# Performance work log

Hardware: AMD Instinct MI355X
Metric: run time of the kernel (lower is better)

Reference implementation:

```python
import jax, jax.numpy as jnp
import numpy as np

NUM_HEADS = 8
NG = 8  # group/grid size: seq = NG**3 = 512


def setup_inputs() -> dict:
    key = jax.random.key(0)
    k1, k2, k3 = jax.random.split(key, 3)
    batch, seq, chan = 32, NG ** 3, 512
    subspace_dim = 24
    x = jax.random.normal(k1, (batch, seq, chan), jnp.float32)
    # fixed symmetric-subspace basis (the free variable `conv_kernel` in the source)
    basis = jax.random.normal(k2, (seq, subspace_dim), jnp.float32)
    # learned param: (subspace_dim, num_heads), init stddev 0.01
    kernel = jax.random.normal(k3, (subspace_dim, NUM_HEADS), jnp.float32) * 0.01
    return {"x": x, "basis": basis, "kernel": kernel}


def reference(x, basis, kernel):
    batch, seq, chan = x.shape
    h, ng = NUM_HEADS, NG
    kn = 2 * ng - 1  # 15: circular tiling window
    ch = chan // h
    # 'batch (8 8 8) (ch h) -> h (batch ch) 8 8 8'
    x_im = x.reshape(batch, ng, ng, ng, ch, h)
    x_im = jnp.transpose(x_im, (5, 0, 4, 1, 2, 3)).reshape(h, batch * ch, ng, ng, ng)
    # circular tiling: tile 2x2x2 then crop to 2*ng-1 per axis; add trailing C=1
    x_im = jnp.tile(x_im, (1, 1, 2, 2, 2))[:, :, :kn, :kn, :kn, None]
    # expand subspace kernel: '(n n n) s, s h -> h n n n 1 1'
    kexp = jnp.einsum('gs,sh->hg', basis, kernel).reshape(h, ng, ng, ng, 1, 1)

    def conv(lhs, rhs):
        return jax.lax.conv_general_dilated(
            lhs, rhs, window_strides=(1, 1, 1), padding='VALID',
            dimension_numbers=('NXYZC', 'XYZIO', 'NXYZC'))

    # per-head VALID conv: [batch*ch, 15,15,15, 1] * [8,8,8,1,1] -> [batch*ch, 8,8,8, 1]
    out = jax.vmap(conv)(x_im, kexp)[..., 0]  # [h, batch*ch, 8, 8, 8]
    # 'h (batch ch) n n n -> batch (n n n) (ch h)'
    out = out.reshape(h, batch, ch, seq)
    out = jnp.transpose(out, (1, 3, 2, 0)).reshape(batch, seq, chan)
    return out
```

## Files before the change

### kernel.cpp

```cpp
#include <hip/hip_runtime.h>


#define S2C 0.70710678118654752f
#define S2  18
#define S1  146
#define CST 1172

template <bool INV>
__device__ __forceinline__ void dft8(float* R, float* I)
{
    float t0r = R[0] + R[4], t0i = I[0] + I[4];
    float t1r = R[1] + R[5], t1i = I[1] + I[5];
    float t2r = R[2] + R[6], t2i = I[2] + I[6];
    float t3r = R[3] + R[7], t3i = I[3] + I[7];
    float b0r = R[0] - R[4], b0i = I[0] - I[4];
    float d1r = R[1] - R[5], d1i = I[1] - I[5];
    float d2r = R[2] - R[6], d2i = I[2] - I[6];
    float d3r = R[3] - R[7], d3i = I[3] - I[7];
    float b1r, b1i, b2r, b2i, b3r, b3i;
    if (!INV) {
        b1r = (d1r + d1i) * S2C;  b1i = (d1i - d1r) * S2C;
        b2r = d2i;                b2i = -d2r;
        b3r = (d3i - d3r) * S2C;  b3i = -(d3r + d3i) * S2C;
    } else {
        b1r = (d1r - d1i) * S2C;  b1i = (d1i + d1r) * S2C;
        b2r = -d2i;               b2i = d2r;
        b3r = -(d3r + d3i) * S2C; b3i = (d3r - d3i) * S2C;
    }
    float u0r = t0r + t2r, u0i = t0i + t2i;
    float u1r = t1r + t3r, u1i = t1i + t3i;
    float u2r = t0r - t2r, u2i = t0i - t2i;
    float e3r = t1r - t3r, e3i = t1i - t3i;
    float u3r, u3i;
    if (!INV) { u3r = e3i;  u3i = -e3r; }
    else      { u3r = -e3i; u3i = e3r;  }
    R[0] = u0r + u1r; I[0] = u0i + u1i;
    R[4] = u0r - u1r; I[4] = u0i - u1i;
    R[2] = u2r + u3r; I[2] = u2i + u3i;
    R[6] = u2r - u3r; I[6] = u2i - u3i;
    float v0r = b0r + b2r, v0i = b0i + b2i;
    float v1r = b1r + b3r, v1i = b1i + b3i;
    float v2r = b0r - b2r, v2i = b0i - b2i;
    float w3r = b1r - b3r, w3i = b1i - b3i;
    float v3r, v3i;
    if (!INV) { v3r = w3i;  v3i = -w3r; }
    else      { v3r = -w3i; v3i = w3r;  }
    R[1] = v0r + v1r; I[1] = v0i + v1i;
    R[5] = v0r - v1r; I[5] = v0i - v1i;
    R[3] = v2r + v3r; I[3] = v2i + v3i;
    R[7] = v2r - v3r; I[7] = v2i - v3i;
}

__device__ const float CTAB8[8] = {1.f, S2C, 0.f, -S2C, -1.f, -S2C, 0.f, S2C};
__device__ const float STAB8[8] = {0.f, S2C, 1.f, S2C, 0.f, -S2C, -1.f, -S2C};

__global__ __launch_bounds__(256)
void eqfft_prep(const float* __restrict__ basis,
                const float* __restrict__ kparam,
                float2* __restrict__ V)
{
    __shared__ float Wl[512];
    __shared__ float CT[8], ST[8];
    const int tid = threadIdx.x;
    const int blk = blockIdx.x;
    const int h   = blk >> 4;
    if (tid < 8) { CT[tid] = CTAB8[tid]; ST[tid] = STAB8[tid]; }
    #pragma unroll
    for (int t = 0; t < 2; ++t) {
        const int g = tid * 2 + t;
        const float* bp = basis + g * 24;
        float acc = 0.f;
        #pragma unroll
        for (int s = 0; s < 24; ++s) acc += bp[s] * kparam[s * 8 + h];
        Wl[(g & 63) * 8 + (g >> 6)] = acc;
    }
    __syncthreads();
    const int f  = (blk & 15) * 32 + (tid >> 3);
    const int g1 = tid & 7;
    const int f1 = f >> 6, f2 = (f >> 3) & 7, f3 = f & 7;
    const int kb = (f1 * g1) & 7;
    float pr = 0.f, pi = 0.f;
    for (int g2 = 0; g2 < 8; ++g2) {
        const int k2 = kb + f2 * g2;
        const float* wrow = &Wl[g2 * 64 + g1];
        #pragma unroll
        for (int g3 = 0; g3 < 8; ++g3) {
            const int k = (k2 + f3 * g3) & 7;
            const float w = wrow[g3 * 8];
            pr += w * CT[k];
            pi += w * ST[k];
        }
    }
    pr += __shfl_xor(pr, 1); pi += __shfl_xor(pi, 1);
    pr += __shfl_xor(pr, 2); pi += __shfl_xor(pi, 2);
    pr += __shfl_xor(pr, 4); pi += __shfl_xor(pi, 4);
    if (g1 == 0)
        V[h * 512 + f] = make_float2(pr * (1.f / 512.f), pi * (1.f / 512.f));
}

__global__ __launch_bounds__(256, 4)
void eqfft_main(const float* __restrict__ x,
                const float2* __restrict__ V,
                float* __restrict__ out)
{
    __shared__ __align__(16) float lds[8 * CST];

    const int tid = threadIdx.x;
    const int bid = blockIdx.x;
    const int b   = bid >> 5;
    const int c0  = (bid & 31) * 16;

    const float* xb = x   + (size_t)b * 262144 + c0;
    float*       ob = out + (size_t)b * 262144 + c0;

    #pragma unroll
    for (int t = 0; t < 4; ++t) {
        const int G = t * 256 + tid;
        const int p = G >> 1;
        const int u = G & 1;
        const float4 A  = *(const float4*)(xb + p * 512 + u * 4);
        const float4 Bv = *(const float4*)(xb + p * 512 + u * 4 + 8);
        const int base = (p >> 6) * S1 + ((p >> 3) & 7) * S2 + (p & 7) * 2;
        float* dst = lds + (u * 4) * CST + base;
        *(float2*)(dst + 0 * CST) = make_float2(A.x, Bv.x);
        *(float2*)(dst + 1 * CST) = make_float2(A.y, Bv.y);
        *(float2*)(dst + 2 * CST) = make_float2(A.z, Bv.z);
        *(float2*)(dst + 3 * CST) = make_float2(A.w, Bv.w);
    }
    __syncthreads();

    const int q = tid >> 5;
    const int e = tid & 31;
    float R0[8], I0[8], R1[8], I1[8];

    {
        const int P0 = 2 * e, P1 = 2 * e + 1;
        float* pa = lds + q * CST + (P0 >> 3) * S1 + (P0 & 7) * S2;
        float* pb = lds + q * CST + (P1 >> 3) * S1 + (P1 & 7) * S2;
        #pragma unroll
        for (int j = 0; j < 8; ++j) {
            const float2 za = *(const float2*)(pa + 2 * j);
            const float2 zb = *(const float2*)(pb + 2 * j);
            R0[j] = za.x; I0[j] = za.y; R1[j] = zb.x; I1[j] = zb.y;
        }
        dft8<false>(R0, I0); dft8<false>(R1, I1);
        #pragma unroll
        for (int j = 0; j < 8; ++j) {
            *(float2*)(pa + 2 * j) = make_float2(R0[j], I0[j]);
            *(float2*)(pb + 2 * j) = make_float2(R1[j], I1[j]);
        }
    }
    __syncthreads();

    {
        const int P0 = 2 * e, P1 = 2 * e + 1;
        float* pa = lds + q * CST + (P0 >> 3) * S1 + (P0 & 7) * 2;
        float* pb = lds + q * CST + (P1 >> 3) * S1 + (P1 & 7) * 2;
        #pragma unroll
        for (int j = 0; j < 8; ++j) {
            const float2 za = *(const float2*)(pa + S2 * j);
            const float2 zb = *(const float2*)(pb + S2 * j);
            R0[j] = za.x; I0[j] = za.y; R1[j] = zb.x; I1[j] = zb.y;
        }
        dft8<false>(R0, I0); dft8<false>(R1, I1);
        #pragma unroll
        for (int j = 0; j < 8; ++j) {
            *(float2*)(pa + S2 * j) = make_float2(R0[j], I0[j]);
            *(float2*)(pb + S2 * j) = make_float2(R1[j], I1[j]);
        }
    }
    __syncthreads();

    {
        const int P0 = 2 * e, P1 = 2 * e + 1;
        const int p2a = P0 >> 3, p3a = P0 & 7;
        const int p2b = P1 >> 3, p3b = P1 & 7;
        const float2* v0 = V + q * 512 + p2a * 8 + p3a;
        const float2* v1 = V + q * 512 + p2b * 8 + p3b;
        float2 va[8], vb[8];
        #pragma unroll
        for (int j = 0; j < 8; ++j) { va[j] = v0[j << 6]; vb[j] = v1[j << 6]; }

        float* pa = lds + q * CST + p2a * S2 + p3a * 2;
        float* pb = lds + q * CST + p2b * S2 + p3b * 2;
        #pragma unroll
        for (int j = 0; j < 8; ++j) {
            const float2 za = *(const float2*)(pa + S1 * j);
            const float2 zb = *(const float2*)(pb + S1 * j);
            R0[j] = za.x; I0[j] = za.y; R1[j] = zb.x; I1[j] = zb.y;
        }
        dft8<false>(R0, I0); dft8<false>(R1, I1);
        #pragma unroll
        for (int j = 0; j < 8; ++j) {
            float nr = R0[j] * va[j].x - I0[j] * va[j].y;
            I0[j]    = R0[j] * va[j].y + I0[j] * va[j].x;
            R0[j]    = nr;
            nr       = R1[j] * vb[j].x - I1[j] * vb[j].y;
            I1[j]    = R1[j] * vb[j].y + I1[j] * vb[j].x;
            R1[j]    = nr;
        }
        dft8<true>(R0, I0); dft8<true>(R1, I1);
        #pragma unroll
        for (int j = 0; j < 8; ++j) {
            *(float2*)(pa + S1 * j) = make_float2(R0[j], I0[j]);
            *(float2*)(pb + S1 * j) = make_float2(R1[j], I1[j]);
        }
    }
    __syncthreads();

    {
        const int P0 = 2 * e, P1 = 2 * e + 1;
        float* pa = lds + q * CST + (P0 >> 3) * S1 + (P0 & 7) * 2;
        float* pb = lds + q * CST + (P1 >> 3) * S1 + (P1 & 7) * 2;
        #pragma unroll
        for (int j = 0; j < 8; ++j) {
            const float2 za = *(const float2*)(pa + S2 * j);
            const float2 zb = *(const float2*)(pb + S2 * j);
            R0[j] = za.x; I0[j] = za.y; R1[j] = zb.x; I1[j] = zb.y;
        }
        dft8<true>(R0, I0); dft8<true>(R1, I1);
        #pragma unroll
        for (int j = 0; j < 8; ++j) {
            *(float2*)(pa + S2 * j) = make_float2(R0[j], I0[j]);
            *(float2*)(pb + S2 * j) = make_float2(R1[j], I1[j]);
        }
    }
    __syncthreads();

    {
        const int P0 = 2 * e, P1 = 2 * e + 1;
        float* pa = lds + q * CST + (P0 >> 3) * S1 + (P0 & 7) * S2;
        float* pb = lds + q * CST + (P1 >> 3) * S1 + (P1 & 7) * S2;
        #pragma unroll
        for (int j = 0; j < 8; ++j) {
            const float2 za = *(const float2*)(pa + 2 * j);
            const float2 zb = *(const float2*)(pb + 2 * j);
            R0[j] = za.x; I0[j] = za.y; R1[j] = zb.x; I1[j] = zb.y;
        }
        dft8<true>(R0, I0); dft8<true>(R1, I1);
        #pragma unroll
        for (int j = 0; j < 8; ++j) {
            *(float2*)(pa + 2 * j) = make_float2(R0[j], I0[j]);
            *(float2*)(pb + 2 * j) = make_float2(R1[j], I1[j]);
        }
    }
    __syncthreads();

    #pragma unroll
    for (int t = 0; t < 4; ++t) {
        const int G = t * 256 + tid;
        const int p = G >> 1;
        const int u = G & 1;
        const int base = (p >> 6) * S1 + ((p >> 3) & 7) * S2 + (p & 7) * 2;
        const float* src = lds + (u * 4) * CST + base;
        const float2 z0 = *(const float2*)(src + 0 * CST);
        const float2 z1 = *(const float2*)(src + 1 * CST);
        const float2 z2 = *(const float2*)(src + 2 * CST);
        const float2 z3 = *(const float2*)(src + 3 * CST);
        *(float4*)(ob + p * 512 + u * 4)     = make_float4(z0.x, z1.x, z2.x, z3.x);
        *(float4*)(ob + p * 512 + u * 4 + 8) = make_float4(z0.y, z1.y, z2.y, z3.y);
    }
}

extern "C" void kernel_launch(void* const* d_in, const int* in_sizes, int n_in,
                              void* d_out, int out_size, void* d_ws, size_t ws_size,
                              hipStream_t stream)
{
    const float* x      = (const float*)d_in[0];
    const float* basis  = (const float*)d_in[1];
    const float* kparam = (const float*)d_in[2];
    float* out          = (float*)d_out;
    float2* V           = (float2*)d_ws;

    hipLaunchKernelGGL(eqfft_prep, dim3(128),  dim3(256), 0, stream, basis, kparam, V);
    hipLaunchKernelGGL(eqfft_main, dim3(1024), dim3(256), 0, stream, x, V, out);
}
```

Baseline: 99.74 us.

## Replace LDS-staged 3D FFT axis transposes with in-wavefront shuffle exchanges

Each wavefront now owns one full 8x8x8 complex volume per pass, with one point per lane. Between the FFT axes, data is exchanged through XOR lane shuffles (a butterfly transpose) instead of LDS round trips separated by __syncthreads. This removes four block barriers and most of the LDS traffic in the middle stages. In exchange it adds many cross-lane shuffle and select instructions, and each wave now handles two volumes one after the other instead of two points of each volume in parallel.

```diff
diff --git a/kernel.cpp b/kernel.cpp
--- a/kernel.cpp
+++ b/kernel.cpp
@@ -51,6 +51,25 @@
     R[7] = v2r - v3r; I[7] = v2i - v3i;
 }
 
+template <int HB, int LM>
+__device__ __forceinline__ void xstage(float* zr, float* zi, int lane)
+{
+    const bool sel = (lane & LM) != 0;
+    #pragma unroll
+    for (int j0 = 0; j0 < 8; ++j0) {
+        if (j0 & HB) continue;
+        const int j1 = j0 | HB;
+        float sr = sel ? zr[j0] : zr[j1];
+        float si = sel ? zi[j0] : zi[j1];
+        sr = __shfl_xor(sr, LM, 64);
+        si = __shfl_xor(si, LM, 64);
+        zr[j0] = sel ? sr : zr[j0];
+        zi[j0] = sel ? si : zi[j0];
+        zr[j1] = sel ? zr[j1] : sr;
+        zi[j1] = sel ? zi[j1] : si;
+    }
+}
+
 __device__ const float CTAB8[8] = {1.f, S2C, 0.f, -S2C, -1.f, -S2C, 0.f, S2C};
 __device__ const float STAB8[8] = {0.f, S2C, 1.f, S2C, 0.f, -S2C, -1.f, -S2C};
 
@@ -129,120 +148,48 @@
     }
     __syncthreads();
 
-    const int q = tid >> 5;
-    const int e = tid & 31;
-    float R0[8], I0[8], R1[8], I1[8];
-
-    {
-        const int P0 = 2 * e, P1 = 2 * e + 1;
-        float* pa = lds + q * CST + (P0 >> 3) * S1 + (P0 & 7) * S2;
-        float* pb = lds + q * CST + (P1 >> 3) * S1 + (P1 & 7) * S2;
+    const int lane = tid & 63;
+    const int wid  = tid >> 6;
+
+    #pragma unroll
+    for (int cc = 0; cc < 2; ++cc) {
+        const int q = wid * 2 + cc;
+        float zr[8], zi[8];
+        float* pp = lds + q * CST + (lane >> 3) * S1 + (lane & 7) * S2;
         #pragma unroll
         for (int j = 0; j < 8; ++j) {
-            const float2 za = *(const float2*)(pa + 2 * j);
-            const float2 zb = *(const float2*)(pb + 2 * j);
-            R0[j] = za.x; I0[j] = za.y; R1[j] = zb.x; I1[j] = zb.y;
+            const float2 z = *(const float2*)(pp + 2 * j);
+            zr[j] = z.x; zi[j] = z.y;
         }
-        dft8<false>(R0, I0); dft8<false>(R1, I1);
+        dft8<false>(zr, zi);
+        xstage<1, 1>(zr, zi, lane);
+        xstage<2, 2>(zr, zi, lane);
+        xstage<4, 4>(zr, zi, lane);
+        dft8<false>(zr, zi);
+        xstage<1, 8>(zr, zi, lane);
+        xstage<2, 16>(zr, zi, lane);
+        xstage<4, 32>(zr, zi, lane);
+        dft8<false>(zr, zi);
+        const float2* vp = V + q * 512 + lane;
         #pragma unroll
         for (int j = 0; j < 8; ++j) {
-            *(float2*)(pa + 2 * j) = make_float2(R0[j], I0[j]);
-            *(float2*)(pb + 2 * j) = make_float2(R1[j], I1[j]);
+            const float2 v = vp[j * 64];
+            const float nr = zr[j] * v.x - zi[j] * v.y;
+            zi[j] = zr[j] * v.y + zi[j] * v.x;
+            zr[j] = nr;
         }
-    }
-    __syncthreads();
-
-    {
-        const int P0 = 2 * e, P1 = 2 * e + 1;
-        float* pa = lds + q * CST + (P0 >> 3) * S1 + (P0 & 7) * 2;
-        float* pb = lds + q * CST + (P1 >> 3) * S1 + (P1 & 7) * 2;
-        #pragma unroll
-        for (int j = 0; j < 8; ++j) {
-            const float2 za = *(const float2*)(pa + S2 * j);
-            const float2 zb = *(const float2*)(pb + S2 * j);
-            R0[j] = za.x; I0[j] = za.y; R1[j] = zb.x; I1[j] = zb.y;
-        }
-        dft8<false>(R0, I0); dft8<false>(R1, I1);
-        #pragma unroll
-        for (int j = 0; j < 8; ++j) {
-            *(float2*)(pa + S2 * j) = make_float2(R0[j], I0[j]);
-            *(float2*)(pb + S2 * j) = make_float2(R1[j], I1[j]);
-        }
-    }
-    __syncthreads();
-
-    {
-        const int P0 = 2 * e, P1 = 2 * e + 1;
-        const int p2a = P0 >> 3, p3a = P0 & 7;
-        const int p2b = P1 >> 3, p3b = P1 & 7;
-        const float2* v0 = V + q * 512 + p2a * 8 + p3a;
-        const float2* v1 = V + q * 512 + p2b * 8 + p3b;
-        float2 va[8], vb[8];
-        #pragma unroll
-        for (int j = 0; j < 8; ++j) { va[j] = v0[j << 6]; vb[j] = v1[j << 6]; }
-
-        float* pa = lds + q * CST + p2a * S2 + p3a * 2;
-        float* pb = lds + q * CST + p2b * S2 + p3b * 2;
-        #pragma unroll
-        for (int j = 0; j < 8; ++j) {
-            const float2 za = *(const float2*)(pa + S1 * j);
-            const float2 zb = *(const float2*)(pb + S1 * j);
-            R0[j] = za.x; I0[j] = za.y; R1[j] = zb.x; I1[j] = zb.y;
-        }
-        dft8<false>(R0, I0); dft8<false>(R1, I1);
-        #pragma unroll
-        for (int j = 0; j < 8; ++j) {
-            float nr = R0[j] * va[j].x - I0[j] * va[j].y;
-            I0[j]    = R0[j] * va[j].y + I0[j] * va[j].x;
-            R0[j]    = nr;
-            nr       = R1[j] * vb[j].x - I1[j] * vb[j].y;
-            I1[j]    = R1[j] * vb[j].y + I1[j] * vb[j].x;
-            R1[j]    = nr;
-        }
-        dft8<true>(R0, I0); dft8<true>(R1, I1);
-        #pragma unroll
-        for (int j = 0; j < 8; ++j) {
-            *(float2*)(pa + S1 * j) = make_float2(R0[j], I0[j]);
-            *(float2*)(pb + S1 * j) = make_float2(R1[j], I1[j]);
-        }
-    }
-    __syncthreads();
-
-    {
-        const int P0 = 2 * e, P1 = 2 * e + 1;
-        float* pa = lds + q * CST + (P0 >> 3) * S1 + (P0 & 7) * 2;
-        float* pb = lds + q * CST + (P1 >> 3) * S1 + (P1 & 7) * 2;
-        #pragma unroll
-        for (int j = 0; j < 8; ++j) {
-            const float2 za = *(const float2*)(pa + S2 * j);
-            const float2 zb = *(const float2*)(pb + S2 * j);
-            R0[j] = za.x; I0[j] = za.y; R1[j] = zb.x; I1[j] = zb.y;
-        }
-        dft8<true>(R0, I0); dft8<true>(R1, I1);
-        #pragma unroll
-        for (int j = 0; j < 8; ++j) {
-            *(float2*)(pa + S2 * j) = make_float2(R0[j], I0[j]);
-            *(float2*)(pb + S2 * j) = make_float2(R1[j], I1[j]);
-        }
-    }
-    __syncthreads();
-
-    {
-        const int P0 = 2 * e, P1 = 2 * e + 1;
-        float* pa = lds + q * CST + (P0 >> 3) * S1 + (P0 & 7) * S2;
-        float* pb = lds + q * CST + (P1 >> 3) * S1 + (P1 & 7) * S2;
-        #pragma unroll
-        for (int j = 0; j < 8; ++j) {
-            const float2 za = *(const float2*)(pa + 2 * j);
-            const float2 zb = *(const float2*)(pb + 2 * j);
-            R0[j] = za.x; I0[j] = za.y; R1[j] = zb.x; I1[j] = zb.y;
-        }
-        dft8<true>(R0, I0); dft8<true>(R1, I1);
-        #pragma unroll
-        for (int j = 0; j < 8; ++j) {
-            *(float2*)(pa + 2 * j) = make_float2(R0[j], I0[j]);
-            *(float2*)(pb + 2 * j) = make_float2(R1[j], I1[j]);
-        }
+        dft8<true>(zr, zi);
+        xstage<1, 8>(zr, zi, lane);
+        xstage<2, 16>(zr, zi, lane);
+        xstage<4, 32>(zr, zi, lane);
+        dft8<true>(zr, zi);
+        xstage<1, 1>(zr, zi, lane);
+        xstage<2, 2>(zr, zi, lane);
+        xstage<4, 4>(zr, zi, lane);
+        dft8<true>(zr, zi);
+        #pragma unroll
+        for (int j = 0; j < 8; ++j)
+            *(float2*)(pp + 2 * j) = make_float2(zr[j], zi[j]);
     }
     __syncthreads();
 
```

After: 112.9 us. +13.2%, slower.
